# Kernel tuning notes

Hardware: AMD Instinct MI355X
Metric: run time of the kernel (lower is better)

The kernel has to match this reference:

```python
import jax, jax.numpy as jnp
import numpy as np

B, N, C = 2, 4096, 512
NUM_HEADS = 8
HEAD_DIM = C // NUM_HEADS
SCALE = HEAD_DIM ** -0.5
THETA = 10000.0


def setup_inputs() -> dict:
    key = jax.random.key(0)
    ks = jax.random.split(key, 5)
    x = jax.random.normal(ks[0], (B, N, C), dtype=jnp.float32)
    Wqkv = jax.random.normal(ks[1], (3 * C, C), dtype=jnp.float32) * 0.02
    bqkv = jax.random.normal(ks[2], (3 * C,), dtype=jnp.float32) * 0.02
    Wproj = jax.random.normal(ks[3], (C, C), dtype=jnp.float32) * 0.02
    bproj = jax.random.normal(ks[4], (C,), dtype=jnp.float32) * 0.02
    return {"x": x, "Wqkv": Wqkv, "bqkv": bqkv, "Wproj": Wproj, "bproj": bproj}


def _rope(x, seq_len, head_dim):
    # x: [B, H, N, head_dim]; interleaved rotary embedding
    freqs = 1.0 / THETA ** (jnp.arange(0, head_dim, 2, dtype=jnp.float32) / head_dim)  # [hd/2]
    t = jnp.arange(seq_len, dtype=jnp.float32)
    freqs_cis = jnp.outer(t, freqs)                      # [N, hd/2]
    sin_f = jnp.sin(freqs_cis)
    cos_f = jnp.cos(freqs_cis)
    x_even = x[..., ::2]                                 # [B, H, N, hd/2]
    x_odd = x[..., 1::2]
    rot = jnp.stack(
        [x_even * cos_f - x_odd * sin_f,
         x_even * sin_f + x_odd * cos_f],
        axis=-1,
    )                                                    # [B, H, N, hd/2, 2]
    return rot.reshape(x.shape)


def reference(x, Wqkv, bqkv, Wproj, bproj):
    b, n, c = x.shape
    # fused QKV projection: y = x @ W.T + b
    qkv = x @ Wqkv.T + bqkv                              # [B, N, 3C]
    qkv = qkv.reshape(b, n, 3, NUM_HEADS, HEAD_DIM)
    qkv = jnp.transpose(qkv, (2, 0, 3, 1, 4))            # [3, B, H, N, hd]
    q, k, v = qkv[0], qkv[1], qkv[2]
    q = _rope(q, n, HEAD_DIM)
    k = _rope(k, n, HEAD_DIM)
    attn = jnp.einsum('bhqd,bhkd->bhqk', q, k) * SCALE   # [B, H, N, N]
    attn = jax.nn.softmax(attn, axis=-1)
    out = jnp.einsum('bhqk,bhkd->bhqd', attn, v)         # [B, H, N, hd]
    out = jnp.transpose(out, (0, 2, 1, 3)).reshape(b, n, c)
    return out @ Wproj.T + bproj
```

## Files before the change

### kernel.cpp

```cpp
#include <hip/hip_runtime.h>
#include <hip/hip_bf16.h>
#include <stdint.h>

#define B_ 2
#define N_ 4096
#define C_ 512
#define H_ 8
#define D_ 64
#define M_ (B_*N_)
#define K3_ (3*C_)
#define NCH 4

typedef __attribute__((ext_vector_type(8)))  short short8;
typedef __attribute__((ext_vector_type(4)))  float f32x4;
typedef __attribute__((ext_vector_type(16))) float f32x16;

static __device__ __forceinline__ unsigned short f2bf(float f) {
  union { float f; unsigned u; } cv; cv.f = f;
  unsigned r = cv.u + 0x7fffu + ((cv.u >> 16) & 1u);
  return (unsigned short)(r >> 16);
}
static __device__ __forceinline__ float bf2f(short x) {
  union { unsigned u; float f; } cv;
  cv.u = ((unsigned)(unsigned short)x) << 16;
  return cv.f;
}
static __device__ __forceinline__ float fexp2(float x) {
#if __has_builtin(__builtin_amdgcn_exp2f)
  return __builtin_amdgcn_exp2f(x);
#else
  return exp2f(x);
#endif
}
static __device__ __forceinline__ unsigned cvt_pk_bf16(float a, float b) {
  unsigned r;
  asm("v_cvt_pk_bf16_f32 %0, %1, %2" : "=v"(r) : "v"(a), "v"(b));
  return r;
}
static __device__ __forceinline__ void gload_lds16(const void* g, void* l) {
  __builtin_amdgcn_global_load_lds((const __attribute__((address_space(1))) unsigned*)g,
                                   (__attribute__((address_space(3))) unsigned*)l, 16, 0, 0);
}
static __device__ __forceinline__ f32x16 zero16() {
  f32x16 z;
#pragma unroll
  for (int i = 0; i < 16; i++) z[i] = 0.f;
  return z;
}

__global__ void prep(const float* __restrict__ x, const float* __restrict__ Wqkv,
                     const float* __restrict__ Wproj,
                     short* __restrict__ xb, short* __restrict__ wqkvb,
                     short* __restrict__ wprjb, float2* __restrict__ tab) {
  int blk = blockIdx.x, t = threadIdx.x;
  if (blk < 4096) {
    int i = blk * 256 + t;
    float4 v = ((const float4*)x)[i];
    short4 o;
    o.x = (short)f2bf(v.x); o.y = (short)f2bf(v.y);
    o.z = (short)f2bf(v.z); o.w = (short)f2bf(v.w);
    ((short4*)xb)[i] = o;
  } else if (blk < 4864) {
    int i = (blk - 4096) * 256 + t;
    float4 v = ((const float4*)Wqkv)[i];
    short4 o;
    o.x = (short)f2bf(v.x); o.y = (short)f2bf(v.y);
    o.z = (short)f2bf(v.z); o.w = (short)f2bf(v.w);
    ((short4*)wqkvb)[i] = o;
  } else if (blk < 5120) {
    int i = (blk - 4864) * 256 + t;
    float4 v = ((const float4*)Wproj)[i];
    short4 o;
    o.x = (short)f2bf(v.x); o.y = (short)f2bf(v.y);
    o.z = (short)f2bf(v.z); o.w = (short)f2bf(v.w);
    ((short4*)wprjb)[i] = o;
  } else {
    int i = (blk - 5120) * 256 + t;
    int p = i & 31, n = i >> 5;
    float freq = exp2f(-((float)(2 * p) / 64.0f) * 13.287712379549449f);
    float ang = (float)n * freq;
    float s, c;
    sincosf(ang, &s, &c);
    float2 r; r.x = c; r.y = s;
    tab[i] = r;
  }
}

__global__ void rope_vt(const short* __restrict__ qkvb, const float2* __restrict__ tab,
                        short* __restrict__ Qf, short* __restrict__ Kf,
                        short* __restrict__ Vf) {
  __shared__ short tile[32][72];
  int blk = blockIdx.x, t = threadIdx.x;
  if (blk < 4096) {
    int idx = blk * 256 + t;
    int lane  = idx & 63;
    int f     = (idx >> 6) & 3;
    int nblk  = (idx >> 8) & 127;
    int h     = (idx >> 15) & 7;
    int b     = (idx >> 18) & 1;
    int tk    = idx >> 19;
    int c = lane & 31, hi = lane >> 5;
    int n = nblk * 32 + c;
    int d0 = f * 16 + hi * 8;
    short8 v = *(const short8*)(qkvb + (size_t)(b * N_ + n) * K3_ + tk * C_ + h * D_ + d0);
    const float2* tp = tab + n * 32 + (d0 >> 1);
    float sc = (tk == 0) ? 0.18033688011112042f : 1.0f;
    short8 w;
#pragma unroll
    for (int j = 0; j < 4; j++) {
      float e = bf2f(v[2 * j]), o = bf2f(v[2 * j + 1]);
      float2 cs = tp[j];
      float e2 = (e * cs.x - o * cs.y) * sc;
      float o2 = (e * cs.y + o * cs.x) * sc;
      w[2 * j] = (short)f2bf(e2);
      w[2 * j + 1] = (short)f2bf(o2);
    }
    short* dst = (tk ? Kf : Qf) + (((size_t)((b * H_ + h) * 128 + nblk) * 4 + f) * 512) + lane * 8;
    *(short8*)dst = w;
  } else {
    int blk2 = blk - 4096;
    int bh = blk2 >> 7, kblk = blk2 & 127;
    int b = bh >> 3, h = bh & 7;
    int n0 = kblk * 32;
    {
      int row = t >> 3, c8 = t & 7;
      short8 v = *(const short8*)(qkvb + (size_t)(b * N_ + n0 + row) * K3_ + 2 * C_ + h * D_ + c8 * 8);
      *(short8*)&tile[row][c8 * 8] = v;
    }
    __syncthreads();
    {
      int frag = t >> 6, lane = t & 63;
      int hi = lane >> 5, c = lane & 31;
      int g = frag & 1, dblk = frag >> 1;
      short8 w;
#pragma unroll
      for (int j = 0; j < 8; j++) w[j] = tile[g * 16 + hi * 8 + j][dblk * 32 + c];
      *(short8*)(Vf + ((size_t)(bh * 128 + kblk) * 4 + frag) * 512 + lane * 8) = w;
    }
  }
}

template<int OUTF32>
__global__ __launch_bounds__(256) void gemm_bt(const short* __restrict__ A, const short* __restrict__ Bw,
                                               const float* __restrict__ bias, void* __restrict__ Cout,
                                               int M, int Nout, int K) {
  __shared__ short As[128 * 32];
  __shared__ short Bs[128 * 32];
  int t = threadIdx.x, lane = t & 63, w = t >> 6, wr = w >> 1, wc = w & 1;
  int tM = blockIdx.x * 128, tN = blockIdx.y * 128;
  int lrow = lane & 15, lhi = lane >> 4;
  f32x4 acc[4][4];
#pragma unroll
  for (int fm = 0; fm < 4; fm++)
#pragma unroll
    for (int fn = 0; fn < 4; fn++)
#pragma unroll
      for (int r = 0; r < 4; r++) acc[fm][fn][r] = 0.f;

  int srow = t >> 2, sq = (t & 3) * 8;
  const short* Ag0 = A  + (size_t)(tM + srow) * K + sq;
  const short* Ag1 = A  + (size_t)(tM + 64 + srow) * K + sq;
  const short* Bg0 = Bw + (size_t)(tN + srow) * K + sq;
  const short* Bg1 = Bw + (size_t)(tN + 64 + srow) * K + sq;
  short* Al0 = As + t * 8;          short* Al1 = As + 2048 + t * 8;
  short* Bl0 = Bs + t * 8;          short* Bl1 = Bs + 2048 + t * 8;

  for (int k0 = 0; k0 < K; k0 += 32) {
    gload_lds16(Ag0 + k0, Al0);
    gload_lds16(Ag1 + k0, Al1);
    gload_lds16(Bg0 + k0, Bl0);
    gload_lds16(Bg1 + k0, Bl1);
    __syncthreads();
    short8 af[4], bfr[4];
#pragma unroll
    for (int f = 0; f < 4; f++) {
      af[f]  = *(const short8*)(As + (wr * 64 + f * 16 + lrow) * 32 + lhi * 8);
      bfr[f] = *(const short8*)(Bs + (wc * 64 + f * 16 + lrow) * 32 + lhi * 8);
    }
#pragma unroll
    for (int fm = 0; fm < 4; fm++)
#pragma unroll
      for (int fn = 0; fn < 4; fn++)
        acc[fm][fn] = __builtin_amdgcn_mfma_f32_16x16x32_bf16(af[fm], bfr[fn], acc[fm][fn], 0, 0, 0);
    __syncthreads();
  }

#pragma unroll
  for (int fn = 0; fn < 4; fn++) {
    int col = tN + wc * 64 + fn * 16 + lrow;
    float bv = bias[col];
#pragma unroll
    for (int fm = 0; fm < 4; fm++) {
      int row0 = tM + wr * 64 + fm * 16 + lhi * 4;
#pragma unroll
      for (int r = 0; r < 4; r++) {
        float v = acc[fm][fn][r] + bv;
        if (OUTF32) ((float*)Cout)[(size_t)(row0 + r) * Nout + col] = v;
        else        ((short*)Cout)[(size_t)(row0 + r) * Nout + col] = (short)f2bf(v);
      }
    }
  }
}

static __device__ __forceinline__ void ld4(short8* dst, const short* p) {
#pragma unroll
  for (int f = 0; f < 4; f++) dst[f] = *(const short8*)(p + f * 512);
}
static __device__ __forceinline__ f32x16 qk4(const short8* k, const short8* q, const f32x16& z0) {
  __builtin_amdgcn_s_setprio(1);
  f32x16 st = __builtin_amdgcn_mfma_f32_32x32x16_bf16(k[0], q[0], z0, 0, 0, 0);
  st = __builtin_amdgcn_mfma_f32_32x32x16_bf16(k[1], q[1], st, 0, 0, 0);
  st = __builtin_amdgcn_mfma_f32_32x32x16_bf16(k[2], q[2], st, 0, 0, 0);
  st = __builtin_amdgcn_mfma_f32_32x32x16_bf16(k[3], q[3], st, 0, 0, 0);
  __builtin_amdgcn_s_setprio(0);
  return st;
}
static __device__ __forceinline__ void soft_pv(const f32x16& st, const short8* v,
                                               f32x16& o0, f32x16& o1, float& lsum) {
  float ls = 0.f;
  unsigned cpk[8];
#pragma unroll
  for (int q2 = 0; q2 < 4; q2++) {
    float e0 = fexp2(st[4 * q2]),     e1 = fexp2(st[4 * q2 + 1]);
    float e2 = fexp2(st[4 * q2 + 2]), e3 = fexp2(st[4 * q2 + 3]);
    ls += (e0 + e1) + (e2 + e3);
    cpk[2 * q2]     = cvt_pk_bf16(e0, e1);
    cpk[2 * q2 + 1] = cvt_pk_bf16(e2, e3);
  }
  lsum += ls;
  unsigned w00 = cpk[0], w02 = cpk[2];
  asm volatile("v_permlane32_swap_b32 %0, %1" : "+v"(w00), "+v"(w02));
  unsigned w01 = cpk[1], w03 = cpk[3];
  asm volatile("v_permlane32_swap_b32 %0, %1" : "+v"(w01), "+v"(w03));
  unsigned w10 = cpk[4], w12 = cpk[6];
  asm volatile("v_permlane32_swap_b32 %0, %1" : "+v"(w10), "+v"(w12));
  unsigned w11 = cpk[5], w13 = cpk[7];
  asm volatile("v_permlane32_swap_b32 %0, %1" : "+v"(w11), "+v"(w13));
  union { unsigned u[4]; short8 s; } u0, u1;
  u0.u[0] = w00; u0.u[1] = w01; u0.u[2] = w02; u0.u[3] = w03;
  u1.u[0] = w10; u1.u[1] = w11; u1.u[2] = w12; u1.u[3] = w13;
  __builtin_amdgcn_s_setprio(1);
  o0 = __builtin_amdgcn_mfma_f32_32x32x16_bf16(u0.s, v[0], o0, 0, 0, 0);
  o0 = __builtin_amdgcn_mfma_f32_32x32x16_bf16(u1.s, v[1], o0, 0, 0, 0);
  o1 = __builtin_amdgcn_mfma_f32_32x32x16_bf16(u0.s, v[2], o1, 0, 0, 0);
  o1 = __builtin_amdgcn_mfma_f32_32x32x16_bf16(u1.s, v[3], o1, 0, 0, 0);
  __builtin_amdgcn_s_setprio(0);
}

__global__ __launch_bounds__(256, 4) void attn(const short* __restrict__ Qf, const short* __restrict__ Kf,
                                               const short* __restrict__ Vf,
                                               short* __restrict__ Op, float* __restrict__ lp) {
  __shared__ short Ks[2][2048];
  __shared__ short Vs[2][2048];
  int bh = blockIdx.x;
  int ch = blockIdx.z;
  int t = threadIdx.x;
  int wv = t >> 6, lane = t & 63;
  int c = lane & 31, hi = lane >> 5;
  int q0 = blockIdx.y * 128 + wv * 32;
  const int nkb = N_ / (NCH * 32);
  int kb0 = ch * nkb;

  const short* Qb = Qf + ((size_t)(bh * 128 + (q0 >> 5)) * 4) * 512 + lane * 8;
  const short* Kg = Kf + ((size_t)(bh * 128 + kb0) * 4) * 512 + t * 8;
  const short* Vg = Vf + ((size_t)(bh * 128 + kb0) * 4) * 512 + t * 8;

  short8 qf4[4];
  ld4(qf4, Qb);

  const f32x16 z0 = zero16();
  f32x16 o0 = z0, o1 = z0;
  float lsum = 0.f;

  gload_lds16(Kg, &Ks[0][t * 8]);
  gload_lds16(Vg, &Vs[0][t * 8]);
  __syncthreads();

  int buf = 0;
  for (int it = 0; it < nkb; ++it) {
    if (it + 1 < nkb) {
      gload_lds16(Kg + (size_t)(it + 1) * 2048, &Ks[buf ^ 1][t * 8]);
      gload_lds16(Vg + (size_t)(it + 1) * 2048, &Vs[buf ^ 1][t * 8]);
    }
    short8 kf[4], vf[4];
#pragma unroll
    for (int f = 0; f < 4; f++) kf[f] = *(const short8*)&Ks[buf][f * 512 + lane * 8];
#pragma unroll
    for (int f = 0; f < 4; f++) vf[f] = *(const short8*)&Vs[buf][f * 512 + lane * 8];
    f32x16 st = qk4(kf, qf4, z0);
    soft_pv(st, vf, o0, o1, lsum);
    __syncthreads();
    buf ^= 1;
  }

  float lt = lsum + __shfl_xor(lsum, 32);
  if (hi == 0) lp[((size_t)ch * 16 + bh) * N_ + q0 + c] = lt;
  short* obase = Op + ((size_t)ch * 16 + bh) * N_ * D_;
#pragma unroll
  for (int r = 0; r < 16; r++) {
    int ql = (r & 3) + 8 * (r >> 2) + 4 * hi;
    int n = q0 + ql;
    obase[(size_t)n * D_ + c]      = (short)f2bf(o0[r]);
    obase[(size_t)n * D_ + 32 + c] = (short)f2bf(o1[r]);
  }
}

__global__ void combine(const short* __restrict__ Op, const float* __restrict__ lp,
                        short* __restrict__ AO) {
  int i = blockIdx.x * blockDim.x + threadIdx.x;
  if (i >= 16 * N_ * 8) return;
  int d8 = i & 7, q = (i >> 3) & (N_ - 1), bh = i >> 15;
  const size_t chs = (size_t)16 * N_ * D_;
  size_t base = ((size_t)bh * N_ + q) * D_ + d8 * 8;
  float acc[8];
#pragma unroll
  for (int j = 0; j < 8; j++) acc[j] = 0.f;
  float l = 0.f;
#pragma unroll
  for (int chv = 0; chv < NCH; chv++) {
    short8 v = *(const short8*)(Op + chv * chs + base);
#pragma unroll
    for (int j = 0; j < 8; j++) acc[j] += bf2f(v[j]);
    l += lp[((size_t)chv * 16 + bh) * N_ + q];
  }
  float inv = 1.0f / l;
  int bb = bh >> 3, h = bh & 7;
  short8 o;
#pragma unroll
  for (int j = 0; j < 8; j++) o[j] = (short)f2bf(acc[j] * inv);
  *(short8*)(AO + ((size_t)(bb * N_ + q)) * C_ + h * D_ + d8 * 8) = o;
}

extern "C" void kernel_launch(void* const* d_in, const int* in_sizes, int n_in,
                              void* d_out, int out_size, void* d_ws, size_t ws_size,
                              hipStream_t stream) {
  const float* x     = (const float*)d_in[0];
  const float* Wqkv  = (const float*)d_in[1];
  const float* bqkv  = (const float*)d_in[2];
  const float* Wproj = (const float*)d_in[3];
  const float* bproj = (const float*)d_in[4];
  float* out = (float*)d_out;
  char* ws = (char*)d_ws;

  const size_t off_wprjb = 0;
  const size_t off_tab   = 524288;
  const size_t off_q     = 1572864;
  const size_t off_k     = 9961472;
  const size_t off_vt    = 18350080;
  const size_t off_ao    = 26738688;
  const size_t off_xb    = 35127296;
  const size_t off_wqkvb = 43515904;
  const size_t off_qkvb  = 45088768;
  const size_t off_op    = 35127296;
  const size_t off_l     = 68681728;
  if (ws_size < 70254592) return;

  short* xb    = (short*)(ws + off_xb);
  short* wqkvb = (short*)(ws + off_wqkvb);
  short* wprjb = (short*)(ws + off_wprjb);
  short* qkvb  = (short*)(ws + off_qkvb);
  short* Qfp   = (short*)(ws + off_q);
  short* Kfp   = (short*)(ws + off_k);
  short* Vfp   = (short*)(ws + off_vt);
  short* AOp   = (short*)(ws + off_ao);
  float2* tab  = (float2*)(ws + off_tab);
  short* Opp   = (short*)(ws + off_op);
  float* lpp   = (float*)(ws + off_l);

  prep<<<dim3(5632), dim3(256), 0, stream>>>(x, Wqkv, Wproj, xb, wqkvb, wprjb, tab);

  gemm_bt<0><<<dim3(64, 12), dim3(256), 0, stream>>>(xb, wqkvb, bqkv, qkvb, M_, K3_, C_);

  rope_vt<<<dim3(6144), dim3(256), 0, stream>>>(qkvb, tab, Qfp, Kfp, Vfp);

  attn<<<dim3(16, 32, NCH), dim3(256), 0, stream>>>(Qfp, Kfp, Vfp, Opp, lpp);
  combine<<<dim3(2048), dim3(256), 0, stream>>>(Opp, lpp, AOp);

  gemm_bt<1><<<dim3(64, 4), dim3(256), 0, stream>>>(AOp, wprjb, bproj, (void*)out, M_, C_, C_);
}
```

Baseline: 144.9 us.

## Stage RoPE Q/K loads through shared memory and halve attention key chunks

The Q/K RoPE path now has each block cooperatively load a 128-row head tile into shared memory with contiguous row reads, then apply the rotation and write four fragment blocks. This replaces scattered per-thread 16-byte gathers across rows. Separately, the attention split-K chunk count drops from 4 to 2. That roughly halves the partial outputs that combine must reduce, at the cost of fewer attention blocks for parallelism.

```diff
diff --git a/kernel.cpp b/kernel.cpp
--- a/kernel.cpp
+++ b/kernel.cpp
@@ -9,7 +9,7 @@
 #define D_ 64
 #define M_ (B_*N_)
 #define K3_ (3*C_)
-#define NCH 4
+#define NCH 2
 
 typedef __attribute__((ext_vector_type(8)))  short short8;
 typedef __attribute__((ext_vector_type(4)))  float f32x4;
@@ -89,36 +89,46 @@
 __global__ void rope_vt(const short* __restrict__ qkvb, const float2* __restrict__ tab,
                         short* __restrict__ Qf, short* __restrict__ Kf,
                         short* __restrict__ Vf) {
-  __shared__ short tile[32][72];
+  __shared__ short tile[128][72];
   int blk = blockIdx.x, t = threadIdx.x;
-  if (blk < 4096) {
-    int idx = blk * 256 + t;
-    int lane  = idx & 63;
-    int f     = (idx >> 6) & 3;
-    int nblk  = (idx >> 8) & 127;
-    int h     = (idx >> 15) & 7;
-    int b     = (idx >> 18) & 1;
-    int tk    = idx >> 19;
+  if (blk < 1024) {
+    int tk = blk >> 9;
+    int bh = (blk & 511) >> 5;
+    int nb4 = blk & 31;
+    int b = bh >> 3, h = bh & 7;
+    int n0 = nb4 * 128;
+#pragma unroll
+    for (int pass = 0; pass < 4; pass++) {
+      int row = pass * 32 + (t >> 3), chunk = t & 7;
+      short8 v = *(const short8*)(qkvb + (size_t)(b * N_ + n0 + row) * K3_ + tk * C_ + h * D_ + chunk * 8);
+      *(short8*)&tile[row][chunk * 8] = v;
+    }
+    __syncthreads();
+    int lane = t & 63, f = t >> 6;
     int c = lane & 31, hi = lane >> 5;
-    int n = nblk * 32 + c;
     int d0 = f * 16 + hi * 8;
-    short8 v = *(const short8*)(qkvb + (size_t)(b * N_ + n) * K3_ + tk * C_ + h * D_ + d0);
-    const float2* tp = tab + n * 32 + (d0 >> 1);
     float sc = (tk == 0) ? 0.18033688011112042f : 1.0f;
-    short8 w;
-#pragma unroll
-    for (int j = 0; j < 4; j++) {
-      float e = bf2f(v[2 * j]), o = bf2f(v[2 * j + 1]);
-      float2 cs = tp[j];
-      float e2 = (e * cs.x - o * cs.y) * sc;
-      float o2 = (e * cs.y + o * cs.x) * sc;
-      w[2 * j] = (short)f2bf(e2);
-      w[2 * j + 1] = (short)f2bf(o2);
-    }
-    short* dst = (tk ? Kf : Qf) + (((size_t)((b * H_ + h) * 128 + nblk) * 4 + f) * 512) + lane * 8;
-    *(short8*)dst = w;
+    short* base = (tk ? Kf : Qf);
+#pragma unroll
+    for (int i = 0; i < 4; i++) {
+      int n_l = i * 32 + c;
+      short8 v = *(const short8*)&tile[n_l][d0];
+      const float2* tp = tab + (size_t)(n0 + n_l) * 32 + (d0 >> 1);
+      short8 w;
+#pragma unroll
+      for (int j = 0; j < 4; j++) {
+        float e = bf2f(v[2 * j]), o = bf2f(v[2 * j + 1]);
+        float2 cs = tp[j];
+        float e2 = (e * cs.x - o * cs.y) * sc;
+        float o2 = (e * cs.y + o * cs.x) * sc;
+        w[2 * j] = (short)f2bf(e2);
+        w[2 * j + 1] = (short)f2bf(o2);
+      }
+      short* dst = base + (((size_t)(bh * 128 + nb4 * 4 + i) * 4 + f) * 512) + lane * 8;
+      *(short8*)dst = w;
+    }
   } else {
-    int blk2 = blk - 4096;
+    int blk2 = blk - 1024;
     int bh = blk2 >> 7, kblk = blk2 & 127;
     int b = bh >> 3, h = bh & 7;
     int n0 = kblk * 32;
@@ -371,7 +381,7 @@
 
   gemm_bt<0><<<dim3(64, 12), dim3(256), 0, stream>>>(xb, wqkvb, bqkv, qkvb, M_, K3_, C_);
 
-  rope_vt<<<dim3(6144), dim3(256), 0, stream>>>(qkvb, tab, Qfp, Kfp, Vfp);
+  rope_vt<<<dim3(3072), dim3(256), 0, stream>>>(qkvb, tab, Qfp, Kfp, Vfp);
 
   attn<<<dim3(16, 32, NCH), dim3(256), 0, stream>>>(Qfp, Kfp, Vfp, Opp, lpp);
   combine<<<dim3(2048), dim3(256), 0, stream>>>(Opp, lpp, AOp);
```

Measured after the change: 143.6 us. Within noise of the previous version (-0.9%).
